# Kernel tuning notes

Hardware: AMD Instinct MI355X
Metric: run time of the kernel (lower is better)

Reference implementation:

```python
import jax, jax.numpy as jnp
import numpy as np

N, B, T, D = 6, 4, 1024, 768
P = 3            # number of prior phases
H, Dh = 2, 32    # n_heads, head_dim
I = H * Dh       # inner_dim
EPS = 1e-5


def setup_inputs() -> dict:
    key = jax.random.key(0)
    ks = jax.random.split(key, 9)
    current_states = jax.random.normal(ks[0], (N, B, T, D), dtype=jnp.float32)
    history_states = jax.random.normal(ks[1], (P, N, B, T, D), dtype=jnp.float32)
    attention_mask = jax.random.randint(ks[2], (B, T), 0, 2, dtype=jnp.int32)
    # Linear weights stored as [in, out] (transposed nn.Linear weight)
    s = 1.0 / np.sqrt(D)
    Wq = jax.random.uniform(ks[3], (N, D, I), jnp.float32, -s, s)  # per-domain q proj
    Wk = jax.random.uniform(ks[4], (D, I), jnp.float32, -s, s)     # shared k proj
    Wv = jax.random.uniform(ks[5], (D, I), jnp.float32, -s, s)     # shared v proj
    so = 1.0 / np.sqrt(I)
    Wo = jax.random.uniform(ks[6], (N, I, D), jnp.float32, -so, so)  # per-domain out proj
    gamma = jnp.ones((N, D), jnp.float32)   # per-domain LayerNorm weight
    beta = jnp.zeros((N, D), jnp.float32)   # per-domain LayerNorm bias
    return {"current_states": current_states, "history_states": history_states,
            "attention_mask": attention_mask, "Wq": Wq, "Wk": Wk, "Wv": Wv,
            "Wo": Wo, "gamma": gamma, "beta": beta}


def reference(current_states, history_states, attention_mask, Wq, Wk, Wv, Wo, gamma, beta):
    x = current_states                                   # [N,B,T,D]
    # concat prior phases along time per domain: [N,B,P*T,D]
    prior = jnp.transpose(history_states, (1, 2, 0, 3, 4)).reshape(N, B, P * T, D)

    q = jnp.einsum('nbtd,ndi->nbti', x, Wq).reshape(N, B, T, H, Dh).transpose(0, 1, 3, 2, 4)       # [N,B,H,T,Dh]
    k = jnp.einsum('nbsd,di->nbsi', prior, Wk).reshape(N, B, P * T, H, Dh).transpose(0, 1, 3, 2, 4)  # [N,B,H,S,Dh]
    v = jnp.einsum('nbsd,di->nbsi', prior, Wv).reshape(N, B, P * T, H, Dh).transpose(0, 1, 3, 2, 4)

    scale = 1.0 / jnp.sqrt(jnp.float32(Dh))
    scores = jnp.einsum('nbhtd,nbhsd->nbhts', q, k) * scale  # [N,B,H,T,P*T]
    full_mask = jnp.tile(attention_mask.astype(jnp.float32), (1, P))  # [B,P*T]
    bias = (1.0 - full_mask)[None, :, None, None, :] * -10000.0
    attn = jax.nn.softmax(scores + bias, axis=-1)
    o = jnp.einsum('nbhts,nbhsd->nbhtd', attn, v)            # [N,B,H,T,Dh]
    o = o.transpose(0, 1, 3, 2, 4).reshape(N, B, T, I)       # [N,B,T,I]
    o = jnp.einsum('nbti,nid->nbtd', o, Wo)                  # [N,B,T,D]

    y = x + o  # residual (dropout p=0)
    mu = jnp.mean(y, axis=-1, keepdims=True)
    var = jnp.mean(jnp.square(y - mu), axis=-1, keepdims=True)
    out = (y - mu) * jax.lax.rsqrt(var + EPS)
    out = out * gamma[:, None, None, :] + beta[:, None, None, :]
    return out
```

## Files before the change

### kernel.cpp

```cpp
#include <hip/hip_runtime.h>
#include <hip/hip_bf16.h>
#include <math.h>

#define NDOM 6
#define BB 4
#define TT 1024
#define DD 768
#define PP 3
#define HH 2
#define DHH 32
#define II 64
#define SS (PP*TT)
#define NROW (NDOM*BB*TT)
#define NKVROW (NDOM*BB*SS)
#define NSPLIT 4
#define NKVB (NKVROW/64)
#define NQB  (NROW/64)
#define LNEPS 1e-5f

typedef unsigned int uint;
typedef uint  u32x4  __attribute__((ext_vector_type(4)));
typedef int   i32x2  __attribute__((ext_vector_type(2)));
typedef float f32x2  __attribute__((ext_vector_type(2)));
typedef float f32x4  __attribute__((ext_vector_type(4)));
typedef float f32x16 __attribute__((ext_vector_type(16)));
typedef __bf16 bf16x8 __attribute__((ext_vector_type(8)));

__device__ __forceinline__ f32x16 mfma32(u32x4 a, u32x4 b, f32x16 c) {
  return __builtin_amdgcn_mfma_f32_32x32x16_bf16(
      __builtin_bit_cast(bf16x8, a), __builtin_bit_cast(bf16x8, b), c, 0, 0, 0);
}

__device__ __forceinline__ uint pkbf(float a, float b) {
  union { __bf16 h[2]; uint u; } v;
  v.h[0] = (__bf16)a; v.h[1] = (__bf16)b;
  return v.u;
}
__device__ __forceinline__ float b2f(uint u16) {
  union { uint i; float f; } v; v.i = u16 << 16; return v.f;
}

__device__ __forceinline__ void plswap(uint a, uint b, uint& x, uint& y) {
#if __has_builtin(__builtin_amdgcn_permlane32_swap)
  i32x2 r = __builtin_amdgcn_permlane32_swap((int)a, (int)b, false, false);
  x = (uint)r.x; y = (uint)r.y;
#else
  uint sa = __shfl_xor(a, 32), sb = __shfl_xor(b, 32);
  bool h1 = (threadIdx.x & 32) != 0;
  x = h1 ? sb : a;
  y = h1 ? b : sa;
#endif
}

__global__ __launch_bounds__(256) void prep_kernel(
    const int* __restrict__ mask, const float* __restrict__ Wk,
    const float* __restrict__ Wv, const float* __restrict__ Wq,
    const float* __restrict__ Wo,
    __hip_bfloat16* __restrict__ Bkv, __hip_bfloat16* __restrict__ Bq,
    __hip_bfloat16* __restrict__ Bo, float* __restrict__ bias2)
{
  int i = blockIdx.x * 256 + threadIdx.x;
  const int N1 = 128 * 768;
  const int N2 = NDOM * 64 * 768;
  const int N3 = NDOM * 768 * 64;
  if (i < N1) {
    int c = i / 768, k = i % 768;
    float v = (c < 64) ? Wk[k * 64 + c] : Wv[k * 64 + (c - 64)];
    Bkv[i] = __float2bfloat16(v);
  } else if (i < N1 + N2) {
    int j = i - N1;
    int n = j / (64 * 768);
    int rem = j % (64 * 768);
    int c = rem / 768, k = rem % 768;
    Bq[j] = __float2bfloat16(Wq[((size_t)n * 768 + k) * 64 + c]);
  } else if (i < N1 + N2 + N3) {
    int j = i - N1 - N2;
    int n = j / (768 * 64);
    int rem = j % (768 * 64);
    int d = rem / 64, k = rem % 64;
    Bo[j] = __float2bfloat16(Wo[((size_t)n * 64 + k) * 768 + d]);
  } else if (i < N1 + N2 + N3 + BB * SS) {
    int j = i - N1 - N2 - N3;
    int b = j / SS, s = j % SS;
    bias2[j] = (1.0f - (float)mask[b * TT + (s & (TT - 1))]) * (-14426.950408889634f);
  }
}

__global__ __launch_bounds__(256) void qkv_gemm_kernel(
    const float* __restrict__ x, const float* __restrict__ hist,
    const __hip_bfloat16* __restrict__ Bkv, const __hip_bfloat16* __restrict__ Bq,
    __hip_bfloat16* __restrict__ Qo, __hip_bfloat16* __restrict__ Kh,
    __hip_bfloat16* __restrict__ Vt2)
{
  __shared__ uint As[2][64 * 32];
  const int tid = threadIdx.x;
  const int lane = tid & 63, w = tid >> 6;
  const int cl = lane & 31, hi = lane >> 5;
  const int r0 = tid >> 3, oct = tid & 7;

  if (blockIdx.x < NKVB) {
    const int brow = blockIdx.x * 64;
    const int nb = brow / SS;
    const int n = nb >> 2, b = nb & 3;
    const int s0 = brow % SS;
    const int p = s0 / TT, t0 = s0 % TT;
    const float* Asrc = hist + (((size_t)(p * NDOM + n) * BB + b) * TT + t0) * 768;

    float4 a0[2], a1[2];
    auto ldA = [&](int kk) {
#pragma unroll
      for (int g = 0; g < 2; ++g) {
        const float* ap = Asrc + (size_t)(r0 + 32 * g) * 768 + kk * 64 + oct * 8;
        a0[g] = *(const float4*)ap;
        a1[g] = *(const float4*)(ap + 4);
      }
    };

    f32x16 acc0 = {}, acc1 = {};
    ldA(0);
    for (int kk = 0; kk < 12; ++kk) {
      uint* dst = As[kk & 1];
#pragma unroll
      for (int g = 0; g < 2; ++g) {
        int row = r0 + 32 * g;
        u32x4 pk = {pkbf(a0[g].x, a0[g].y), pkbf(a0[g].z, a0[g].w),
                    pkbf(a1[g].x, a1[g].y), pkbf(a1[g].z, a1[g].w)};
        *(u32x4*)&dst[row * 32 + ((oct ^ (row & 7)) << 2)] = pk;
      }
      __syncthreads();
      if (kk + 1 < 12) ldA(kk + 1);
#pragma unroll
      for (int ks = 0; ks < 4; ++ks) {
        int kg = kk * 64 + ks * 16 + hi * 8;
        u32x4 bfrag = *(const u32x4*)(Bkv + (size_t)(w * 32 + cl) * 768 + kg);
        int oc = ks * 2 + hi;
        int ro0 = cl, ro1 = cl + 32;
        u32x4 fa0 = *(const u32x4*)&dst[ro0 * 32 + ((oc ^ (ro0 & 7)) << 2)];
        u32x4 fa1 = *(const u32x4*)&dst[ro1 * 32 + ((oc ^ (ro1 & 7)) << 2)];
        acc0 = mfma32(fa0, bfrag, acc0);
        acc1 = mfma32(fa1, bfrag, acc1);
      }
    }

    if (w < 2) {
      const size_t base = (size_t)(nb * 2 + w) * SS;
#pragma unroll
      for (int r = 0; r < 16; ++r) {
        int rl = (r & 3) + 8 * (r >> 2) + 4 * hi;
        Kh[(base + s0 + rl) * 32 + cl]      = __float2bfloat16(acc0[r]);
        Kh[(base + s0 + 32 + rl) * 32 + cl] = __float2bfloat16(acc1[r]);
      }
    } else {
      const int h = w - 2;
#pragma unroll
      for (int k = 0; k < 4; ++k) {
        int sb0 = (s0 + 8 * k) >> 3;
        int sb1 = sb0 + 4;
        size_t A0 = (((size_t)(nb * 2 + h) * (SS / 8) + sb0) * 32 + cl) * 8 + 4 * hi;
        size_t A1 = (((size_t)(nb * 2 + h) * (SS / 8) + sb1) * 32 + cl) * 8 + 4 * hi;
        *(uint2*)(Vt2 + A0) = uint2{pkbf(acc0[4*k], acc0[4*k+1]), pkbf(acc0[4*k+2], acc0[4*k+3])};
        *(uint2*)(Vt2 + A1) = uint2{pkbf(acc1[4*k], acc1[4*k+1]), pkbf(acc1[4*k+2], acc1[4*k+3])};
      }
    }
  } else {
    const int brow = (blockIdx.x - NKVB) * 64;
    const int n = brow >> 12;
    const int wr = w >> 1, wc = w & 1;
    const float* Asrc = x + (size_t)brow * 768;
    const __hip_bfloat16* Bn = Bq + (size_t)n * 64 * 768;

    float4 a0[2], a1[2];
    auto ldA = [&](int kk) {
#pragma unroll
      for (int g = 0; g < 2; ++g) {
        const float* ap = Asrc + (size_t)(r0 + 32 * g) * 768 + kk * 64 + oct * 8;
        a0[g] = *(const float4*)ap;
        a1[g] = *(const float4*)(ap + 4);
      }
    };

    f32x16 acc = {};
    ldA(0);
    for (int kk = 0; kk < 12; ++kk) {
      uint* dst = As[kk & 1];
#pragma unroll
      for (int g = 0; g < 2; ++g) {
        int row = r0 + 32 * g;
        u32x4 pk = {pkbf(a0[g].x, a0[g].y), pkbf(a0[g].z, a0[g].w),
                    pkbf(a1[g].x, a1[g].y), pkbf(a1[g].z, a1[g].w)};
        *(u32x4*)&dst[row * 32 + ((oct ^ (row & 7)) << 2)] = pk;
      }
      __syncthreads();
      if (kk + 1 < 12) ldA(kk + 1);
#pragma unroll
      for (int ks = 0; ks < 4; ++ks) {
        int kg = kk * 64 + ks * 16 + hi * 8;
        u32x4 bfrag = *(const u32x4*)(Bn + (size_t)(wc * 32 + cl) * 768 + kg);
        int oc = ks * 2 + hi;
        int ro = wr * 32 + cl;
        u32x4 fa = *(const u32x4*)&dst[ro * 32 + ((oc ^ (ro & 7)) << 2)];
        acc = mfma32(fa, bfrag, acc);
      }
    }
    int c = wc * 32 + cl;
#pragma unroll
    for (int r = 0; r < 16; ++r) {
      int rl = (r & 3) + 8 * (r >> 2) + 4 * hi;
      Qo[(size_t)(brow + wr * 32 + rl) * 64 + c] = __float2bfloat16(acc[r]);
    }
  }
}

struct KV { u32x4 k0, k1, k2, k3, v0, v1, v2, v3; };

__global__ __launch_bounds__(256) void attn_kernel(
    const __hip_bfloat16* __restrict__ Q, const __hip_bfloat16* __restrict__ Kh,
    const __hip_bfloat16* __restrict__ Vt2, const float* __restrict__ bias2,
    __hip_bfloat16* __restrict__ Op, float* __restrict__ Mp, float* __restrict__ Lp)
{
  const int tid = threadIdx.x;
  const int lane = tid & 63, w = tid >> 6;
  const int cl = lane & 31, hi = lane >> 5;
  const int bid = blockIdx.x;
  const int g = bid % 48;
  const int rest = bid / 48;
  const int sp = rest >> 3;
  const int tq = rest & 7;
  const int qtile = tq * 4 + w;
  const int h = g & 1, nb = g >> 1;
  const int b = nb & 3;
  const int qrow = nb * TT + qtile * 32;
  const int sbase = sp * (SS / NSPLIT);

  const __hip_bfloat16* Qp = Q + (size_t)(qrow + cl) * 64 + h * 32 + hi * 8;
  u32x4 qf0 = *(const u32x4*)Qp;
  u32x4 qf1 = *(const u32x4*)(Qp + 16);

  const __hip_bfloat16* Kp = Kh + ((size_t)(nb * 2 + h) * SS + sbase) * 32;
  const __hip_bfloat16* Vp = Vt2 + (size_t)(nb * 2 + h) * SS * 32 + (size_t)sbase * 32;
  const float* Bp = bias2 + b * SS + sbase + hi * 4;

  const float scale2 = 0.17677669529663687f * 1.4426950408889634f;
  const f32x2 sc2 = {scale2, scale2};

  f32x16 ot = {};
  float m = -1e30f, lsum = 0.f;

  auto loadKV = [&](int it) {
    KV t;
    const __hip_bfloat16* kp = Kp + (size_t)it * 64 * 32;
    t.k0 = *(const u32x4*)(kp + cl * 32 + hi * 8);
    t.k1 = *(const u32x4*)(kp + cl * 32 + 16 + hi * 8);
    t.k2 = *(const u32x4*)(kp + 1024 + cl * 32 + hi * 8);
    t.k3 = *(const u32x4*)(kp + 1024 + cl * 32 + 16 + hi * 8);
    const __hip_bfloat16* vp = Vp + (size_t)it * 64 * 32;
    t.v0 = *(const u32x4*)(vp + ((0 * 2 + hi) * 32 + cl) * 8);
    t.v1 = *(const u32x4*)(vp + ((1 * 2 + hi) * 32 + cl) * 8);
    t.v2 = *(const u32x4*)(vp + ((2 * 2 + hi) * 32 + cl) * 8);
    t.v3 = *(const u32x4*)(vp + ((3 * 2 + hi) * 32 + cl) * 8);
    return t;
  };

  auto compute = [&](const KV& t, int it) {
    f32x16 pz0 = {}, pz1 = {};
    pz0 = mfma32(t.k0, qf0, pz0);
    pz0 = mfma32(t.k1, qf1, pz0);
    pz1 = mfma32(t.k2, qf0, pz1);
    pz1 = mfma32(t.k3, qf1, pz1);
    const float* bp = Bp + it * 64;
    f32x4 b4[8];
#pragma unroll
    for (int q = 0; q < 8; ++q) b4[q] = *(const f32x4*)(bp + 8 * q);
    f32x2 p2[16];
#pragma unroll
    for (int i = 0; i < 8; ++i) {
      f32x4 bq0 = b4[i >> 1];
      f32x4 bq1 = b4[4 + (i >> 1)];
      f32x2 bv0 = (i & 1) ? f32x2{bq0.z, bq0.w} : f32x2{bq0.x, bq0.y};
      f32x2 bv1 = (i & 1) ? f32x2{bq1.z, bq1.w} : f32x2{bq1.x, bq1.y};
      p2[i]     = f32x2{pz0[2*i], pz0[2*i+1]} * sc2 + bv0;
      p2[8 + i] = f32x2{pz1[2*i], pz1[2*i+1]} * sc2 + bv1;
    }
    f32x2 mx = p2[0];
#pragma unroll
    for (int i = 1; i < 16; ++i) {
      mx.x = fmaxf(mx.x, p2[i].x);
      mx.y = fmaxf(mx.y, p2[i].y);
    }
    float tm = fmaxf(mx.x, mx.y);
    tm = fmaxf(tm, __shfl_xor(tm, 32));
    if (!__all(tm - m <= 8.f)) {
      float mn = fmaxf(m, tm);
      float f = exp2f(m - mn);
#pragma unroll
      for (int i = 0; i < 16; ++i) ot[i] *= f;
      lsum *= f;
      m = mn;
    }
    const f32x2 m2 = {m, m};
    f32x2 s2 = {0.f, 0.f};
#pragma unroll
    for (int i = 0; i < 16; ++i) {
      f32x2 d = p2[i] - m2;
      f32x2 e = {exp2f(d.x), exp2f(d.y)};
      p2[i] = e;
      s2 += e;
    }
    float ts = s2.x + s2.y;
    ts += __shfl_xor(ts, 32);
    lsum += ts;
    uint cv[16];
#pragma unroll
    for (int i = 0; i < 16; ++i) cv[i] = pkbf(p2[i].x, p2[i].y);
    u32x4 pf0, pf1, pf2, pf3;
    {
      uint x0, y0, x1, y1;
      plswap(cv[0], cv[2],  x0, y0); plswap(cv[1], cv[3],  x1, y1);
      pf0 = u32x4{x0, x1, y0, y1};
      plswap(cv[4], cv[6],  x0, y0); plswap(cv[5], cv[7],  x1, y1);
      pf1 = u32x4{x0, x1, y0, y1};
      plswap(cv[8], cv[10], x0, y0); plswap(cv[9], cv[11], x1, y1);
      pf2 = u32x4{x0, x1, y0, y1};
      plswap(cv[12], cv[14], x0, y0); plswap(cv[13], cv[15], x1, y1);
      pf3 = u32x4{x0, x1, y0, y1};
    }
    ot = mfma32(t.v0, pf0, ot);
    ot = mfma32(t.v1, pf1, ot);
    ot = mfma32(t.v2, pf2, ot);
    ot = mfma32(t.v3, pf3, ot);
  };

  KV cur = loadKV(0);
#pragma unroll 1
  for (int it = 0; it < 12; ++it) {
    KV nxt = loadKV(it + 1 < 12 ? it + 1 : 11);
    compute(cur, it);
    cur = nxt;
    __builtin_amdgcn_s_barrier();
  }

  __hip_bfloat16* op = Op + ((size_t)sp * NROW + qrow + cl) * 64 + h * 32 + 4 * hi;
#pragma unroll
  for (int k = 0; k < 4; ++k) {
    uint2 wv = {pkbf(ot[4*k], ot[4*k+1]), pkbf(ot[4*k+2], ot[4*k+3])};
    *(uint2*)(op + 8 * k) = wv;
  }
  if (lane < 32) {
    int mi = ((sp * 24 + nb) * 2 + h) * TT + qtile * 32 + cl;
    Mp[mi] = m;
    Lp[mi] = lsum;
  }
}

__global__ __launch_bounds__(256) void oproj_ln_kernel(
    const float* __restrict__ x, const __hip_bfloat16* __restrict__ Op,
    const float* __restrict__ Mp, const float* __restrict__ Lp,
    const __hip_bfloat16* __restrict__ Bo, const float* __restrict__ gamma,
    const float* __restrict__ beta, float* __restrict__ out)
{
  __shared__ float red[4][32][2];
  __shared__ float redf[32][2];
  const int tid = threadIdx.x;
  const int lane = tid & 63, w = tid >> 6;
  const int cl = lane & 31, hi = lane >> 5;
  const int row0 = blockIdx.x * 32;
  const int n = row0 >> 12;
  const int nb = row0 >> 10;
  const int trow = (row0 & 1023) + cl;
  const int MLS = 24 * 2 * TT;

  float wsp[2][NSPLIT];
#pragma unroll
  for (int h = 0; h < 2; ++h) {
    int mi = (nb * 2 + h) * TT + trow;
    float mv[NSPLIT], lv[NSPLIT];
#pragma unroll
    for (int sp = 0; sp < NSPLIT; ++sp) { mv[sp] = Mp[mi + sp * MLS]; lv[sp] = Lp[mi + sp * MLS]; }
    float ms = mv[0];
#pragma unroll
    for (int sp = 1; sp < NSPLIT; ++sp) ms = fmaxf(ms, mv[sp]);
    float den = 0.f;
#pragma unroll
    for (int sp = 0; sp < NSPLIT; ++sp) { wsp[h][sp] = exp2f(mv[sp] - ms); den = fmaf(lv[sp], wsp[h][sp], den); }
    float inv = 1.0f / den;
#pragma unroll
    for (int sp = 0; sp < NSPLIT; ++sp) wsp[h][sp] *= inv;
  }

  u32x4 af[4];
#pragma unroll
  for (int ks = 0; ks < 4; ++ks) {
    int h = ks >> 1;
    size_t off = (size_t)(row0 + cl) * 64 + ks * 16 + hi * 8;
    f32x2 s0 = {}, s1 = {}, s2 = {}, s3 = {};
#pragma unroll
    for (int sp = 0; sp < NSPLIT; ++sp) {
      u32x4 v = *(const u32x4*)(Op + (size_t)sp * NROW * 64 + off);
      float wv = wsp[h][sp];
      s0 += f32x2{b2f(v[0] & 0xffffu), b2f(v[0] >> 16)} * wv;
      s1 += f32x2{b2f(v[1] & 0xffffu), b2f(v[1] >> 16)} * wv;
      s2 += f32x2{b2f(v[2] & 0xffffu), b2f(v[2] >> 16)} * wv;
      s3 += f32x2{b2f(v[3] & 0xffffu), b2f(v[3] >> 16)} * wv;
    }
    af[ks] = u32x4{pkbf(s0.x, s0.y), pkbf(s1.x, s1.y), pkbf(s2.x, s2.y), pkbf(s3.x, s3.y)};
  }

  const __hip_bfloat16* Bp = Bo + ((size_t)n * 768 + w * 192 + cl) * 64 + hi * 8;
  f32x16 acc[6] = {};
#pragma unroll
  for (int ks = 0; ks < 4; ++ks) {
#pragma unroll
    for (int t = 0; t < 6; ++t) {
      u32x4 bb = *(const u32x4*)(Bp + (size_t)(t * 32) * 64 + ks * 16);
      acc[t] = mfma32(af[ks], bb, acc[t]);
    }
  }

  float s1[16], s2[16];
#pragma unroll
  for (int r = 0; r < 16; ++r) { s1[r] = 0.f; s2[r] = 0.f; }
#pragma unroll
  for (int t = 0; t < 6; ++t) {
#pragma unroll
    for (int r = 0; r < 16; ++r) {
      int R = (r & 3) + 8 * (r >> 2) + 4 * hi;
      int col = w * 192 + t * 32 + cl;
      float y = acc[t][r] + x[(size_t)(row0 + R) * 768 + col];
      acc[t][r] = y;
      s1[r] += y;
      s2[r] = fmaf(y, y, s2[r]);
    }
  }
#pragma unroll
  for (int r = 0; r < 16; ++r) {
#pragma unroll
    for (int off = 1; off < 32; off <<= 1) {
      s1[r] += __shfl_xor(s1[r], off);
      s2[r] += __shfl_xor(s2[r], off);
    }
  }
  if (cl == 0) {
#pragma unroll
    for (int r = 0; r < 16; ++r) {
      int R = (r & 3) + 8 * (r >> 2) + 4 * hi;
      red[w][R][0] = s1[r];
      red[w][R][1] = s2[r];
    }
  }
  __syncthreads();
  if (tid < 64) {
    int R = tid & 31, st = tid >> 5;
    redf[R][st] = red[0][R][st] + red[1][R][st] + red[2][R][st] + red[3][R][st];
  }
  __syncthreads();

  float gv[6], bv[6];
#pragma unroll
  for (int t = 0; t < 6; ++t) {
    int col = w * 192 + t * 32 + cl;
    gv[t] = gamma[n * 768 + col];
    bv[t] = beta[n * 768 + col];
  }
#pragma unroll
  for (int r = 0; r < 16; ++r) {
    int R = (r & 3) + 8 * (r >> 2) + 4 * hi;
    float mu = redf[R][0] * (1.0f / 768.0f);
    float var = redf[R][1] * (1.0f / 768.0f) - mu * mu;
    float rs = rsqrtf(var + LNEPS);
#pragma unroll
    for (int t = 0; t < 6; ++t) {
      int col = w * 192 + t * 32 + cl;
      out[(size_t)(row0 + R) * 768 + col] = (acc[t][r] - mu) * rs * gv[t] + bv[t];
    }
  }
}

extern "C" void kernel_launch(void* const* d_in, const int* in_sizes, int n_in,
                              void* d_out, int out_size, void* d_ws, size_t ws_size,
                              hipStream_t stream) {
  const float* x     = (const float*)d_in[0];
  const float* hist  = (const float*)d_in[1];
  const int*   mask  = (const int*)d_in[2];
  const float* Wq    = (const float*)d_in[3];
  const float* Wk    = (const float*)d_in[4];
  const float* Wv    = (const float*)d_in[5];
  const float* Wo    = (const float*)d_in[6];
  const float* gamma = (const float*)d_in[7];
  const float* beta  = (const float*)d_in[8];
  float* out = (float*)d_out;

  char* ws = (char*)d_ws;
  __hip_bfloat16* Qb  = (__hip_bfloat16*)ws;  ws += (size_t)NROW * II * 2;
  __hip_bfloat16* Kh  = (__hip_bfloat16*)ws;  ws += (size_t)NKVROW * II * 2;
  __hip_bfloat16* Vt2 = (__hip_bfloat16*)ws;  ws += (size_t)NKVROW * II * 2;
  __hip_bfloat16* Op  = (__hip_bfloat16*)ws;  ws += (size_t)NSPLIT * NROW * II * 2;
  float* Mp           = (float*)ws;           ws += (size_t)NSPLIT * 24 * 2 * TT * 4;
  float* Lp           = (float*)ws;           ws += (size_t)NSPLIT * 24 * 2 * TT * 4;
  __hip_bfloat16* Bkv = (__hip_bfloat16*)ws;  ws += (size_t)128 * 768 * 2;
  __hip_bfloat16* Bq  = (__hip_bfloat16*)ws;  ws += (size_t)NDOM * 64 * 768 * 2;
  __hip_bfloat16* Bo  = (__hip_bfloat16*)ws;  ws += (size_t)NDOM * 768 * 64 * 2;
  float* bias2        = (float*)ws;           ws += (size_t)BB * SS * 4;

  const int PREP_N = 128*768 + NDOM*64*768 + NDOM*768*64 + BB*SS;
  prep_kernel<<<(PREP_N + 255) / 256, 256, 0, stream>>>(mask, Wk, Wv, Wq, Wo, Bkv, Bq, Bo, bias2);
  qkv_gemm_kernel<<<NKVB + NQB, 256, 0, stream>>>(x, hist, Bkv, Bq, Qb, Kh, Vt2);
  attn_kernel<<<48 * 8 * NSPLIT, 256, 0, stream>>>(Qb, Kh, Vt2, bias2, Op, Mp, Lp);
  oproj_ln_kernel<<<NROW / 32, 256, 0, stream>>>(x, Op, Mp, Lp, Bo, gamma, beta, out);
}
```

Measured before the change: 219.2 us.

## Restructure QKV GEMM to 32-row tiles with full-K LDS staging and fragment-ordered weights

The QKV projection now uses 32-row blocks that load the whole 768-wide fp32 row slab at once, convert it to bf16 into a single swizzled LDS buffer, and run the full K loop after one barrier. The per-step double-buffered loads and barriers are gone. Weights are pre-packed in MFMA fragment order so each lane's B load is contiguous, and two accumulators alternate to break the MFMA dependency chain. This doubles the block count for more parallelism and fewer syncs, but uses 48KB of LDS per block, which can lower occupancy. It also leaves half the waves idle in the Q blocks.

```diff
diff --git a/kernel.cpp b/kernel.cpp
--- a/kernel.cpp
+++ b/kernel.cpp
@@ -14,8 +14,8 @@
 #define NROW (NDOM*BB*TT)
 #define NKVROW (NDOM*BB*SS)
 #define NSPLIT 4
-#define NKVB (NKVROW/64)
-#define NQB  (NROW/64)
+#define NKVB (NKVROW/32)
+#define NQB  (NROW/32)
 #define LNEPS 1e-5f
 
 typedef unsigned int uint;
@@ -56,23 +56,24 @@
     const int* __restrict__ mask, const float* __restrict__ Wk,
     const float* __restrict__ Wv, const float* __restrict__ Wq,
     const float* __restrict__ Wo,
-    __hip_bfloat16* __restrict__ Bkv, __hip_bfloat16* __restrict__ Bq,
+    __hip_bfloat16* __restrict__ Bkvf, __hip_bfloat16* __restrict__ Bqf,
     __hip_bfloat16* __restrict__ Bo, float* __restrict__ bias2)
 {
   int i = blockIdx.x * 256 + threadIdx.x;
-  const int N1 = 128 * 768;
-  const int N2 = NDOM * 64 * 768;
+  const int N1 = 96 * 128 * 8;
+  const int N2 = NDOM * 96 * 64 * 8;
   const int N3 = NDOM * 768 * 64;
   if (i < N1) {
-    int c = i / 768, k = i % 768;
+    int e = i & 7, c = (i >> 3) & 127, slot = i >> 10;
+    int k = (slot >> 1) * 16 + (slot & 1) * 8 + e;
     float v = (c < 64) ? Wk[k * 64 + c] : Wv[k * 64 + (c - 64)];
-    Bkv[i] = __float2bfloat16(v);
+    Bkvf[i] = __float2bfloat16(v);
   } else if (i < N1 + N2) {
     int j = i - N1;
-    int n = j / (64 * 768);
-    int rem = j % (64 * 768);
-    int c = rem / 768, k = rem % 768;
-    Bq[j] = __float2bfloat16(Wq[((size_t)n * 768 + k) * 64 + c]);
+    int n = j / 49152, rem = j % 49152;
+    int e = rem & 7, c = (rem >> 3) & 63, slot = rem >> 9;
+    int k = (slot >> 1) * 16 + (slot & 1) * 8 + e;
+    Bqf[j] = __float2bfloat16(Wq[((size_t)n * 768 + k) * 64 + c]);
   } else if (i < N1 + N2 + N3) {
     int j = i - N1 - N2;
     int n = j / (768 * 64);
@@ -88,125 +89,99 @@
 
 __global__ __launch_bounds__(256) void qkv_gemm_kernel(
     const float* __restrict__ x, const float* __restrict__ hist,
-    const __hip_bfloat16* __restrict__ Bkv, const __hip_bfloat16* __restrict__ Bq,
+    const __hip_bfloat16* __restrict__ Bkvf, const __hip_bfloat16* __restrict__ Bqf,
     __hip_bfloat16* __restrict__ Qo, __hip_bfloat16* __restrict__ Kh,
     __hip_bfloat16* __restrict__ Vt2)
 {
-  __shared__ uint As[2][64 * 32];
+  __shared__ uint As[12288];
   const int tid = threadIdx.x;
   const int lane = tid & 63, w = tid >> 6;
   const int cl = lane & 31, hi = lane >> 5;
-  const int r0 = tid >> 3, oct = tid & 7;
-
-  if (blockIdx.x < NKVB) {
-    const int brow = blockIdx.x * 64;
-    const int nb = brow / SS;
-    const int n = nb >> 2, b = nb & 3;
-    const int s0 = brow % SS;
-    const int p = s0 / TT, t0 = s0 % TT;
-    const float* Asrc = hist + (((size_t)(p * NDOM + n) * BB + b) * TT + t0) * 768;
-
-    float4 a0[2], a1[2];
-    auto ldA = [&](int kk) {
-#pragma unroll
-      for (int g = 0; g < 2; ++g) {
-        const float* ap = Asrc + (size_t)(r0 + 32 * g) * 768 + kk * 64 + oct * 8;
-        a0[g] = *(const float4*)ap;
-        a1[g] = *(const float4*)(ap + 4);
+  const int row = tid >> 3, oct = tid & 7;
+
+  const bool isKV = blockIdx.x < NKVB;
+  const float* Asrc;
+  int nb = 0, s0 = 0, n = 0, brow = 0;
+  if (isKV) {
+    brow = blockIdx.x * 32;
+    nb = brow / SS; n = nb >> 2;
+    int b = nb & 3;
+    s0 = brow % SS;
+    int p = s0 / TT, t0 = s0 % TT;
+    Asrc = hist + (((size_t)(p * NDOM + n) * BB + b) * TT + t0) * 768;
+  } else {
+    brow = (blockIdx.x - NKVB) * 32;
+    n = brow >> 12;
+    Asrc = x + (size_t)brow * 768;
+  }
+
+  {
+    const float* src = Asrc + (size_t)row * 768;
+    f32x4 fb[12];
+#pragma unroll
+    for (int half = 0; half < 2; ++half) {
+#pragma unroll
+      for (int j = 0; j < 6; ++j) {
+        int s = oct + 8 * (half * 6 + j);
+        fb[2 * j]     = *(const f32x4*)(src + s * 8);
+        fb[2 * j + 1] = *(const f32x4*)(src + s * 8 + 4);
       }
-    };
-
-    f32x16 acc0 = {}, acc1 = {};
-    ldA(0);
-    for (int kk = 0; kk < 12; ++kk) {
-      uint* dst = As[kk & 1];
-#pragma unroll
-      for (int g = 0; g < 2; ++g) {
-        int row = r0 + 32 * g;
-        u32x4 pk = {pkbf(a0[g].x, a0[g].y), pkbf(a0[g].z, a0[g].w),
-                    pkbf(a1[g].x, a1[g].y), pkbf(a1[g].z, a1[g].w)};
-        *(u32x4*)&dst[row * 32 + ((oct ^ (row & 7)) << 2)] = pk;
+#pragma unroll
+      for (int j = 0; j < 6; ++j) {
+        int s = oct + 8 * (half * 6 + j);
+        int sw = (s & ~15) | ((s & 15) ^ (row & 15));
+        *(u32x4*)&As[row * 384 + sw * 4] =
+            u32x4{pkbf(fb[2*j].x, fb[2*j].y), pkbf(fb[2*j].z, fb[2*j].w),
+                  pkbf(fb[2*j+1].x, fb[2*j+1].y), pkbf(fb[2*j+1].z, fb[2*j+1].w)};
       }
-      __syncthreads();
-      if (kk + 1 < 12) ldA(kk + 1);
-#pragma unroll
-      for (int ks = 0; ks < 4; ++ks) {
-        int kg = kk * 64 + ks * 16 + hi * 8;
-        u32x4 bfrag = *(const u32x4*)(Bkv + (size_t)(w * 32 + cl) * 768 + kg);
-        int oc = ks * 2 + hi;
-        int ro0 = cl, ro1 = cl + 32;
-        u32x4 fa0 = *(const u32x4*)&dst[ro0 * 32 + ((oc ^ (ro0 & 7)) << 2)];
-        u32x4 fa1 = *(const u32x4*)&dst[ro1 * 32 + ((oc ^ (ro1 & 7)) << 2)];
-        acc0 = mfma32(fa0, bfrag, acc0);
-        acc1 = mfma32(fa1, bfrag, acc1);
-      }
-    }
-
+    }
+  }
+  __syncthreads();
+
+  if (isKV) {
+    const __hip_bfloat16* bb = Bkvf + (size_t)(w * 32 + cl) * 8;
+    f32x16 aE = {}, aO = {};
+#pragma unroll 4
+    for (int ks = 0; ks < 48; ++ks) {
+      int slot = ks * 2 + hi;
+      int sw = (slot & ~15) | ((slot & 15) ^ (cl & 15));
+      u32x4 a = *(const u32x4*)&As[cl * 384 + sw * 4];
+      u32x4 b = *(const u32x4*)(bb + (size_t)slot * 128 * 8);
+      if (ks & 1) aO = mfma32(a, b, aO); else aE = mfma32(a, b, aE);
+    }
+    f32x16 acc = aE + aO;
     if (w < 2) {
-      const size_t base = (size_t)(nb * 2 + w) * SS;
+      size_t base = (size_t)(nb * 2 + w) * SS;
 #pragma unroll
       for (int r = 0; r < 16; ++r) {
         int rl = (r & 3) + 8 * (r >> 2) + 4 * hi;
-        Kh[(base + s0 + rl) * 32 + cl]      = __float2bfloat16(acc0[r]);
-        Kh[(base + s0 + 32 + rl) * 32 + cl] = __float2bfloat16(acc1[r]);
+        Kh[(base + s0 + rl) * 32 + cl] = __float2bfloat16(acc[r]);
       }
     } else {
-      const int h = w - 2;
+      int h = w - 2;
 #pragma unroll
       for (int k = 0; k < 4; ++k) {
-        int sb0 = (s0 + 8 * k) >> 3;
-        int sb1 = sb0 + 4;
-        size_t A0 = (((size_t)(nb * 2 + h) * (SS / 8) + sb0) * 32 + cl) * 8 + 4 * hi;
-        size_t A1 = (((size_t)(nb * 2 + h) * (SS / 8) + sb1) * 32 + cl) * 8 + 4 * hi;
-        *(uint2*)(Vt2 + A0) = uint2{pkbf(acc0[4*k], acc0[4*k+1]), pkbf(acc0[4*k+2], acc0[4*k+3])};
-        *(uint2*)(Vt2 + A1) = uint2{pkbf(acc1[4*k], acc1[4*k+1]), pkbf(acc1[4*k+2], acc1[4*k+3])};
+        int sb = (s0 + 8 * k) >> 3;
+        size_t A0 = (((size_t)(nb * 2 + h) * (SS / 8) + sb) * 32 + cl) * 8 + 4 * hi;
+        *(uint2*)(Vt2 + A0) = uint2{pkbf(acc[4*k], acc[4*k+1]), pkbf(acc[4*k+2], acc[4*k+3])};
       }
     }
-  } else {
-    const int brow = (blockIdx.x - NKVB) * 64;
-    const int n = brow >> 12;
-    const int wr = w >> 1, wc = w & 1;
-    const float* Asrc = x + (size_t)brow * 768;
-    const __hip_bfloat16* Bn = Bq + (size_t)n * 64 * 768;
-
-    float4 a0[2], a1[2];
-    auto ldA = [&](int kk) {
-#pragma unroll
-      for (int g = 0; g < 2; ++g) {
-        const float* ap = Asrc + (size_t)(r0 + 32 * g) * 768 + kk * 64 + oct * 8;
-        a0[g] = *(const float4*)ap;
-        a1[g] = *(const float4*)(ap + 4);
-      }
-    };
-
-    f32x16 acc = {};
-    ldA(0);
-    for (int kk = 0; kk < 12; ++kk) {
-      uint* dst = As[kk & 1];
-#pragma unroll
-      for (int g = 0; g < 2; ++g) {
-        int row = r0 + 32 * g;
-        u32x4 pk = {pkbf(a0[g].x, a0[g].y), pkbf(a0[g].z, a0[g].w),
-                    pkbf(a1[g].x, a1[g].y), pkbf(a1[g].z, a1[g].w)};
-        *(u32x4*)&dst[row * 32 + ((oct ^ (row & 7)) << 2)] = pk;
-      }
-      __syncthreads();
-      if (kk + 1 < 12) ldA(kk + 1);
-#pragma unroll
-      for (int ks = 0; ks < 4; ++ks) {
-        int kg = kk * 64 + ks * 16 + hi * 8;
-        u32x4 bfrag = *(const u32x4*)(Bn + (size_t)(wc * 32 + cl) * 768 + kg);
-        int oc = ks * 2 + hi;
-        int ro = wr * 32 + cl;
-        u32x4 fa = *(const u32x4*)&dst[ro * 32 + ((oc ^ (ro & 7)) << 2)];
-        acc = mfma32(fa, bfrag, acc);
-      }
-    }
-    int c = wc * 32 + cl;
+  } else if (w < 2) {
+    const __hip_bfloat16* bb = Bqf + (size_t)n * 49152 + (size_t)(w * 32 + cl) * 8;
+    f32x16 aE = {}, aO = {};
+#pragma unroll 4
+    for (int ks = 0; ks < 48; ++ks) {
+      int slot = ks * 2 + hi;
+      int sw = (slot & ~15) | ((slot & 15) ^ (cl & 15));
+      u32x4 a = *(const u32x4*)&As[cl * 384 + sw * 4];
+      u32x4 b = *(const u32x4*)(bb + (size_t)slot * 64 * 8);
+      if (ks & 1) aO = mfma32(a, b, aO); else aE = mfma32(a, b, aE);
+    }
+    f32x16 acc = aE + aO;
 #pragma unroll
     for (int r = 0; r < 16; ++r) {
       int rl = (r & 3) + 8 * (r >> 2) + 4 * hi;
-      Qo[(size_t)(brow + wr * 32 + rl) * 64 + c] = __float2bfloat16(acc[r]);
+      Qo[(size_t)(brow + rl) * 64 + w * 32 + cl] = __float2bfloat16(acc[r]);
     }
   }
 }
@@ -496,14 +471,14 @@
   __hip_bfloat16* Op  = (__hip_bfloat16*)ws;  ws += (size_t)NSPLIT * NROW * II * 2;
   float* Mp           = (float*)ws;           ws += (size_t)NSPLIT * 24 * 2 * TT * 4;
   float* Lp           = (float*)ws;           ws += (size_t)NSPLIT * 24 * 2 * TT * 4;
-  __hip_bfloat16* Bkv = (__hip_bfloat16*)ws;  ws += (size_t)128 * 768 * 2;
-  __hip_bfloat16* Bq  = (__hip_bfloat16*)ws;  ws += (size_t)NDOM * 64 * 768 * 2;
+  __hip_bfloat16* Bkvf = (__hip_bfloat16*)ws; ws += (size_t)96 * 128 * 8 * 2;
+  __hip_bfloat16* Bqf  = (__hip_bfloat16*)ws; ws += (size_t)NDOM * 96 * 64 * 8 * 2;
   __hip_bfloat16* Bo  = (__hip_bfloat16*)ws;  ws += (size_t)NDOM * 768 * 64 * 2;
   float* bias2        = (float*)ws;           ws += (size_t)BB * SS * 4;
 
-  const int PREP_N = 128*768 + NDOM*64*768 + NDOM*768*64 + BB*SS;
-  prep_kernel<<<(PREP_N + 255) / 256, 256, 0, stream>>>(mask, Wk, Wv, Wq, Wo, Bkv, Bq, Bo, bias2);
-  qkv_gemm_kernel<<<NKVB + NQB, 256, 0, stream>>>(x, hist, Bkv, Bq, Qb, Kh, Vt2);
+  const int PREP_N = 96*128*8 + NDOM*96*64*8 + NDOM*768*64 + BB*SS;
+  prep_kernel<<<(PREP_N + 255) / 256, 256, 0, stream>>>(mask, Wk, Wv, Wq, Wo, Bkvf, Bqf, Bo, bias2);
+  qkv_gemm_kernel<<<NKVB + NQB, 256, 0, stream>>>(x, hist, Bkvf, Bqf, Qb, Kh, Vt2);
   attn_kernel<<<48 * 8 * NSPLIT, 256, 0, stream>>>(Qb, Kh, Vt2, bias2, Op, Mp, Lp);
   oproj_ln_kernel<<<NROW / 32, 256, 0, stream>>>(x, Op, Mp, Lp, Bo, gamma, beta, out);
 }
```

New measurement: 206.9 us. -5.6%, faster.
